# Kernel optimization log

Measured on AMD Instinct MI355X. Metric: run time of the kernel, lower is better.

## Reference

```python
import jax, jax.numpy as jnp
import numpy as np

N_QUBITS = 8
N_LAYERS = 4
DIM = 2 ** N_QUBITS
C64 = jnp.complex64
ROTS = ['RX', 'RY', 'RZ']

# PauliZ sign table: wire 0 is the most-significant bit (PennyLane convention).
_bits = (np.arange(DIM)[:, None] >> (N_QUBITS - 1 - np.arange(N_QUBITS))[None, :]) & 1
Z_SIGNS = jnp.asarray(1.0 - 2.0 * _bits, dtype=jnp.float32)  # (DIM, n_qubits)


def _apply_1q(state, gate, q):
    """Apply a 2x2 gate (or batched (B,2,2) gate) on qubit q. state: (B, DIM) complex64."""
    L = 2 ** q
    R = DIM // (2 * L)
    s = state.reshape(-1, L, 2, R)
    if gate.ndim == 3:
        s = jnp.einsum('bij,bljr->blir', gate, s)
    else:
        s = jnp.einsum('ij,bljr->blir', gate, s)
    return s.reshape(-1, DIM)


def _apply_cnot(state, q):
    """CNOT with control q, target q+1 (adjacent wires): permute basis states."""
    L = 2 ** q
    R = DIM // (4 * L)
    perm = jnp.array([0, 1, 3, 2])
    s = state.reshape(-1, L, 4, R)[:, :, perm, :]
    return s.reshape(-1, DIM)


def _rot(name, t):
    """Scalar-angle single-qubit rotation gate, 2x2 complex64."""
    h = 0.5 * t
    c = jnp.cos(h).astype(C64)
    s = jnp.sin(h).astype(C64)
    if name == 'RX':
        return jnp.stack([jnp.stack([c, -1j * s]), jnp.stack([-1j * s, c])])
    if name == 'RY':
        return jnp.stack([jnp.stack([c, -s]), jnp.stack([s, c])])
    e = jnp.exp(-1j * h).astype(C64)  # RZ = diag(e^{-it/2}, e^{+it/2})
    z = jnp.zeros((), C64)
    return jnp.stack([jnp.stack([e, z]), jnp.stack([z, jnp.conj(e)])])


def _circuit(enc, theta):
    """enc: (B, n_qubits) real angles; theta: (n_layers, n_qubits, 3). Returns <Z_q>: (B, n_qubits)."""
    B = enc.shape[0]
    state = jnp.zeros((B, DIM), C64).at[:, 0].set(1.0)
    # Angle encoding: RY(enc[:, q]) on each wire (batched gate).
    for q in range(N_QUBITS):
        h = 0.5 * enc[:, q]
        c, s = jnp.cos(h), jnp.sin(h)
        g = jnp.stack([jnp.stack([c, -s], -1), jnp.stack([s, c], -1)], -2).astype(C64)
        state = _apply_1q(state, g, q)
    # PCE ansatz: per layer RX/RY/RZ on every qubit, then brickwall CNOT entanglement.
    for l in range(N_LAYERS):
        for q in range(N_QUBITS):
            for r, name in enumerate(ROTS):
                state = _apply_1q(state, _rot(name, theta[l, q, r]), q)
        for i in range(l % 2, N_QUBITS - 1, 2):
            state = _apply_cnot(state, i)
    probs = state.real ** 2 + state.imag ** 2          # (B, DIM)
    return probs @ Z_SIGNS                              # (B, n_qubits)


def setup_inputs() -> dict:
    key = jax.random.key(0)
    k1, k2, k3, k4 = jax.random.split(key, 4)
    B, D_IN, D_OUT = 8192, 512, 512
    x = jax.random.normal(k1, (B, D_IN), dtype=jnp.float32)
    W_in = jax.random.normal(k2, (N_QUBITS, D_IN), dtype=jnp.float32) * (1.0 / np.sqrt(D_IN))
    W_out = jax.random.normal(k3, (D_OUT, N_QUBITS), dtype=jnp.float32) * (1.0 / np.sqrt(N_QUBITS))
    theta = jax.random.normal(k4, (N_LAYERS, N_QUBITS, 3), dtype=jnp.float32) * 0.1
    return {"x": x, "W_in": W_in, "W_out": W_out, "theta": theta}


def reference(x, W_in, W_out, theta):
    enc = jnp.tanh(x @ W_in.T) * jnp.pi     # (B, n_qubits), encoded angles
    z = _circuit(enc, theta)                # (B, n_qubits), PauliZ expvals
    return z @ W_out.T                      # (B, output_dim)
```

## Files before the change

### kernel.cpp

```cpp
#include <hip/hip_runtime.h>
#include <hip/hip_bf16.h>
#include <math.h>


typedef __attribute__((ext_vector_type(8))) short bf16x8;
typedef __attribute__((ext_vector_type(4))) float f32x4;

__device__ __forceinline__ float2 shfl_xor_f2(float2 v, int m) {
  float2 r;
  r.x = __shfl_xor(v.x, m, 64);
  r.y = __shfl_xor(v.y, m, 64);
  return r;
}
__device__ __forceinline__ float2 cfma(float2 u, float2 v, float2 acc) {
  acc.x = fmaf(u.x, v.x, fmaf(-u.y, v.y, acc.x));
  acc.y = fmaf(u.x, v.y, fmaf(u.y, v.x, acc.y));
  return acc;
}

__device__ __forceinline__ void apply_gate(float2 (&a)[4], int q, float2 u00,
                                           float2 u01, float2 u10, float2 u11,
                                           int lane) {
  const float2 z0 = make_float2(0.f, 0.f);
  if (q == 7) {
    float2 n0 = cfma(u00, a[0], cfma(u01, a[1], z0));
    float2 n1 = cfma(u10, a[0], cfma(u11, a[1], z0));
    float2 n2 = cfma(u00, a[2], cfma(u01, a[3], z0));
    float2 n3 = cfma(u10, a[2], cfma(u11, a[3], z0));
    a[0] = n0; a[1] = n1; a[2] = n2; a[3] = n3;
  } else if (q == 6) {
    float2 n0 = cfma(u00, a[0], cfma(u01, a[2], z0));
    float2 n2 = cfma(u10, a[0], cfma(u11, a[2], z0));
    float2 n1 = cfma(u00, a[1], cfma(u01, a[3], z0));
    float2 n3 = cfma(u10, a[1], cfma(u11, a[3], z0));
    a[0] = n0; a[1] = n1; a[2] = n2; a[3] = n3;
  } else {
    int m = 1 << (5 - q);
    bool b = (lane >> (5 - q)) & 1;
    float2 ca = b ? u11 : u00;
    float2 cp = b ? u10 : u01;
    #pragma unroll
    for (int k = 0; k < 4; ++k) {
      float2 p = shfl_xor_f2(a[k], m);
      a[k] = cfma(ca, a[k], cfma(cp, p, z0));
    }
  }
}

__device__ __forceinline__ void apply_cnot(float2 (&a)[4], int q, int lane) {
  if (q <= 4) {
    int m = 1 << (4 - q);
    bool ctrl = (lane >> (5 - q)) & 1;
    #pragma unroll
    for (int k = 0; k < 4; ++k) {
      float2 p = shfl_xor_f2(a[k], m);
      a[k].x = ctrl ? p.x : a[k].x;
      a[k].y = ctrl ? p.y : a[k].y;
    }
  } else if (q == 5) {
    bool ct = lane & 1;
    float2 n0 = ct ? a[2] : a[0];
    float2 n1 = ct ? a[3] : a[1];
    float2 n2 = ct ? a[0] : a[2];
    float2 n3 = ct ? a[1] : a[3];
    a[0] = n0; a[1] = n1; a[2] = n2; a[3] = n3;
  } else {
    float2 t = a[2]; a[2] = a[3]; a[3] = t;
  }
}

__global__ __launch_bounds__(256) void k01_kernel(
    const float* __restrict__ x, const float* __restrict__ W_in,
    const float* __restrict__ theta, __hip_bfloat16* __restrict__ Bt,
    __hip_bfloat16* __restrict__ psi, int psi_stride, int B) {
  __shared__ float mats[32 * 8];
  const int tid = threadIdx.x;
  const int lane = tid & 63;

  if (blockIdx.x < 64) {
    if (tid < 32) {
      int l = tid >> 3, q = tid & 7;
      const float* th = theta + (l * 8 + q) * 3;
      float h1 = 0.5f * th[0], h2 = 0.5f * th[1], h3 = 0.5f * th[2];
      float c1 = cosf(h1), s1 = sinf(h1);
      float c2 = cosf(h2), s2 = sinf(h2);
      float c3 = cosf(h3), s3 = sinf(h3);
      float m00r = c2 * c1, m00i = s2 * s1;
      float m01r = -s2 * c1, m01i = -c2 * s1;
      float m10r = s2 * c1, m10i = -c2 * s1;
      float m11r = c1 * c2, m11i = -s1 * s2;
      float* o = &mats[tid * 8];
      o[0] = c3 * m00r + s3 * m00i;  o[1] = c3 * m00i - s3 * m00r;
      o[2] = c3 * m01r + s3 * m01i;  o[3] = c3 * m01i - s3 * m01r;
      o[4] = c3 * m10r - s3 * m10i;  o[5] = c3 * m10i + s3 * m10r;
      o[6] = c3 * m11r - s3 * m11i;  o[7] = c3 * m11i + s3 * m11r;
    }
    __syncthreads();

    const int j = blockIdx.x * 4 + (tid >> 6);
    float2 a[4];
    #pragma unroll
    for (int k = 0; k < 4; ++k)
      a[k] = make_float2((lane * 4 + k == j) ? 1.f : 0.f, 0.f);

    #pragma unroll
    for (int l = 0; l < 4; ++l) {
      #pragma unroll
      for (int q = 0; q < 8; ++q) {
        const float* m = &mats[(l * 8 + q) * 8];
        float2 u00 = make_float2(m[0], m[1]);
        float2 u01 = make_float2(m[2], m[3]);
        float2 u10 = make_float2(m[4], m[5]);
        float2 u11 = make_float2(m[6], m[7]);
        apply_gate(a, q, u00, u01, u10, u11, lane);
      }
      #pragma unroll
      for (int i = (l & 1); i < 7; i += 2) apply_cnot(a, i, lane);
    }
    #pragma unroll
    for (int k = 0; k < 4; ++k) {
      int n0 = (lane * 4 + k) * 2;
      Bt[n0 * 256 + j]       = __float2bfloat16(a[k].x);
      Bt[(n0 + 1) * 256 + j] = __float2bfloat16(a[k].y);
    }
    return;
  }

  const int b = (int)(blockIdx.x - 64) * 4 + (tid >> 6);
  if (b >= B) return;

  float xv[8];
  #pragma unroll
  for (int j = 0; j < 8; ++j) xv[j] = x[b * 512 + j * 64 + lane];

  float acc[8];
  #pragma unroll
  for (int q = 0; q < 8; ++q) {
    float s = 0.f;
    #pragma unroll
    for (int j = 0; j < 8; ++j)
      s = fmaf(xv[j], W_in[q * 512 + j * 64 + lane], s);
    acc[q] = s;
  }
  #pragma unroll
  for (int m = 1; m < 64; m <<= 1) {
    #pragma unroll
    for (int q = 0; q < 8; ++q) acc[q] += __shfl_xor(acc[q], m, 64);
  }

  float cq[8], sq[8];
  #pragma unroll
  for (int q = 0; q < 8; ++q) {
    float e  = __expf(2.f * acc[q]);
    float th = 1.f - __fdividef(2.f, e + 1.f);
    float h  = 0.5f * 3.14159265358979323846f * th;
    cq[q] = __cosf(h);
    sq[q] = __sinf(h);
  }

  float base = 1.f;
  #pragma unroll
  for (int q = 0; q < 6; ++q)
    base *= ((lane >> (5 - q)) & 1) ? sq[q] : cq[q];

  float a0 = base * cq[6] * cq[7];
  float a1 = base * cq[6] * sq[7];
  float a2 = base * sq[6] * cq[7];
  float a3 = base * sq[6] * sq[7];

  __hip_bfloat16 h4[4] = {__float2bfloat16(a0), __float2bfloat16(a1),
                          __float2bfloat16(a2), __float2bfloat16(a3)};
  uint2 pk = *reinterpret_cast<uint2*>(h4);
  *reinterpret_cast<uint2*>(psi + (size_t)b * psi_stride + lane * 4) = pk;
}

__global__ __launch_bounds__(256, 1) void k2_kernel(
    const __hip_bfloat16* __restrict__ psi, const __hip_bfloat16* __restrict__ Bt,
    const float* __restrict__ W_out, float* __restrict__ out, int psi_stride) {
  __shared__ float z_lds[4][32][8];
  __shared__ float z_final[32][8];
  const int tid = threadIdx.x;
  const int lane = tid & 63;
  const int w = tid >> 6;
  const int rowbase = blockIdx.x * 32;
  const int cl = lane & 15;
  const int kg = lane >> 4;

  const short* psis = (const short*)psi;
  const short* Bts  = (const short*)Bt;

  bf16x8 Af[2][8];
  #pragma unroll
  for (int rt = 0; rt < 2; ++rt)
    #pragma unroll
    for (int kb = 0; kb < 8; ++kb)
      Af[rt][kb] = *(const bf16x8*)(psis +
          (size_t)(rowbase + rt * 16 + cl) * psi_stride + kb * 32 + kg * 8);

  const int wcol = w * 128;
  f32x4 acc[2][8];
  #pragma unroll
  for (int rt = 0; rt < 2; ++rt)
    #pragma unroll
    for (int ct = 0; ct < 8; ++ct) acc[rt][ct] = (f32x4){0.f, 0.f, 0.f, 0.f};

  #pragma unroll
  for (int ct = 0; ct < 8; ++ct) {
    const short* bp = Bts + (size_t)(wcol + ct * 16 + cl) * 256 + kg * 8;
    bf16x8 Bf[8];
    #pragma unroll
    for (int kb = 0; kb < 8; ++kb) Bf[kb] = *(const bf16x8*)(bp + kb * 32);
    #pragma unroll
    for (int kb = 0; kb < 8; ++kb) {
      acc[0][ct] = __builtin_amdgcn_mfma_f32_16x16x32_bf16(Af[0][kb], Bf[kb],
                                                           acc[0][ct], 0, 0, 0);
      acc[1][ct] = __builtin_amdgcn_mfma_f32_16x16x32_bf16(Af[1][kb], Bf[kb],
                                                           acc[1][ct], 0, 0, 0);
    }
  }

  float zacc[2][4][4];
  #pragma unroll
  for (int rt = 0; rt < 2; ++rt)
    #pragma unroll
    for (int u = 0; u < 4; ++u)
      #pragma unroll
      for (int jr = 0; jr < 4; ++jr) zacc[rt][u][jr] = 0.f;

  #pragma unroll
  for (int ct = 0; ct < 8; ++ct) {
    int n = wcol + ct * 16 + cl;
    int i = n >> 1;
    int ib = (lane & 1) ? (i & 15) : (i >> 4);
    float s[4];
    #pragma unroll
    for (int u = 0; u < 4; ++u)
      s[u] = ((ib >> (3 - u)) & 1) ? -1.f : 1.f;
    #pragma unroll
    for (int rt = 0; rt < 2; ++rt) {
      #pragma unroll
      for (int jr = 0; jr < 4; ++jr) {
        float v = acc[rt][ct][jr];
        v = v * v;
        float P = v + __shfl_xor(v, 1, 64);
        #pragma unroll
        for (int u = 0; u < 4; ++u)
          zacc[rt][u][jr] = fmaf(s[u], P, zacc[rt][u][jr]);
      }
    }
  }

  #pragma unroll
  for (int m = 2; m <= 8; m <<= 1)
    #pragma unroll
    for (int rt = 0; rt < 2; ++rt)
      #pragma unroll
      for (int u = 0; u < 4; ++u)
        #pragma unroll
        for (int jr = 0; jr < 4; ++jr)
          zacc[rt][u][jr] += __shfl_xor(zacc[rt][u][jr], m, 64);

  if (cl <= 1) {
    #pragma unroll
    for (int rt = 0; rt < 2; ++rt)
      #pragma unroll
      for (int u = 0; u < 4; ++u)
        #pragma unroll
        for (int jr = 0; jr < 4; ++jr)
          z_lds[w][rt * 16 + kg * 4 + jr][(lane & 1) * 4 + u] = zacc[rt][u][jr];
  }
  __syncthreads();

  {
    int r = tid >> 3, q = tid & 7;
    z_final[r][q] = z_lds[0][r][q] + z_lds[1][r][q] + z_lds[2][r][q] +
                    z_lds[3][r][q];
  }
  __syncthreads();

  const int o0 = tid, o1 = 256 + tid;
  float4 wa0 = *(const float4*)(W_out + o0 * 8);
  float4 wb0 = *(const float4*)(W_out + o0 * 8 + 4);
  float4 wa1 = *(const float4*)(W_out + o1 * 8);
  float4 wb1 = *(const float4*)(W_out + o1 * 8 + 4);
  #pragma unroll 4
  for (int r = 0; r < 32; ++r) {
    float4 z0 = *(const float4*)&z_final[r][0];
    float4 z1 = *(const float4*)&z_final[r][4];
    float d0 = wa0.x * z0.x + wa0.y * z0.y + wa0.z * z0.z + wa0.w * z0.w +
               wb0.x * z1.x + wb0.y * z1.y + wb0.z * z1.z + wb0.w * z1.w;
    float d1 = wa1.x * z0.x + wa1.y * z0.y + wa1.z * z0.z + wa1.w * z0.w +
               wb1.x * z1.x + wb1.y * z1.y + wb1.z * z1.z + wb1.w * z1.w;
    out[(size_t)(rowbase + r) * 512 + o0] = d0;
    out[(size_t)(rowbase + r) * 512 + o1] = d1;
  }
}

extern "C" void kernel_launch(void* const* d_in, const int* in_sizes, int n_in,
                              void* d_out, int out_size, void* d_ws, size_t ws_size,
                              hipStream_t stream) {
  const float* x     = (const float*)d_in[0];
  const float* W_in  = (const float*)d_in[1];
  const float* W_out = (const float*)d_in[2];
  const float* theta = (const float*)d_in[3];
  float* out = (float*)d_out;

  const int B = in_sizes[0] / 512;
  const size_t btBytes  = 512 * 256 * sizeof(__hip_bfloat16);
  const size_t psiBytes = (size_t)B * 256 * sizeof(__hip_bfloat16);

  __hip_bfloat16* Bt = (__hip_bfloat16*)d_ws;
  __hip_bfloat16* psi;
  int psi_stride;
  if (ws_size >= btBytes + psiBytes) {
    psi = (__hip_bfloat16*)((char*)d_ws + btBytes);
    psi_stride = 256;
  } else {
    psi = (__hip_bfloat16*)d_out;
    psi_stride = 1024;
  }

  hipLaunchKernelGGL(k01_kernel, dim3(64 + B / 4), dim3(256), 0, stream,
                     x, W_in, theta, Bt, psi, psi_stride, B);
  hipLaunchKernelGGL(k2_kernel, dim3(B / 32), dim3(256), 0, stream,
                     psi, Bt, W_out, out, psi_stride);
}
```

Measured before the change: 35.28 us.

## Fuse encoding into MFMA kernel via LDS psi staging, split unitary kernel

The psi encoding (x·W_in, tanh, product state) now runs inside the MFMA kernel and stages psi in a swizzled LDS tile, so psi no longer round-trips through global memory. The unitary build moves to its own small 64-block kernel. Row tiles drop from 32 to 16 per block with launch bounds allowing 2 blocks per SM, and output stores become float2. The trade-off is that each block reloads W_in and B-matrix fragments for fewer rows, and k1 now runs serially before k2 instead of concurrently with the encoding work.

```diff
diff --git a/kernel.cpp b/kernel.cpp
--- a/kernel.cpp
+++ b/kernel.cpp
@@ -69,163 +69,152 @@
   }
 }
 
-__global__ __launch_bounds__(256) void k01_kernel(
-    const float* __restrict__ x, const float* __restrict__ W_in,
-    const float* __restrict__ theta, __hip_bfloat16* __restrict__ Bt,
-    __hip_bfloat16* __restrict__ psi, int psi_stride, int B) {
+__global__ __launch_bounds__(256) void k1_unitary(
+    const float* __restrict__ theta, __hip_bfloat16* __restrict__ Bt) {
   __shared__ float mats[32 * 8];
   const int tid = threadIdx.x;
   const int lane = tid & 63;
 
-  if (blockIdx.x < 64) {
-    if (tid < 32) {
-      int l = tid >> 3, q = tid & 7;
-      const float* th = theta + (l * 8 + q) * 3;
-      float h1 = 0.5f * th[0], h2 = 0.5f * th[1], h3 = 0.5f * th[2];
-      float c1 = cosf(h1), s1 = sinf(h1);
-      float c2 = cosf(h2), s2 = sinf(h2);
-      float c3 = cosf(h3), s3 = sinf(h3);
-      float m00r = c2 * c1, m00i = s2 * s1;
-      float m01r = -s2 * c1, m01i = -c2 * s1;
-      float m10r = s2 * c1, m10i = -c2 * s1;
-      float m11r = c1 * c2, m11i = -s1 * s2;
-      float* o = &mats[tid * 8];
-      o[0] = c3 * m00r + s3 * m00i;  o[1] = c3 * m00i - s3 * m00r;
-      o[2] = c3 * m01r + s3 * m01i;  o[3] = c3 * m01i - s3 * m01r;
-      o[4] = c3 * m10r - s3 * m10i;  o[5] = c3 * m10i + s3 * m10r;
-      o[6] = c3 * m11r - s3 * m11i;  o[7] = c3 * m11i + s3 * m11r;
-    }
-    __syncthreads();
-
-    const int j = blockIdx.x * 4 + (tid >> 6);
-    float2 a[4];
-    #pragma unroll
-    for (int k = 0; k < 4; ++k)
-      a[k] = make_float2((lane * 4 + k == j) ? 1.f : 0.f, 0.f);
-
-    #pragma unroll
-    for (int l = 0; l < 4; ++l) {
-      #pragma unroll
-      for (int q = 0; q < 8; ++q) {
-        const float* m = &mats[(l * 8 + q) * 8];
-        float2 u00 = make_float2(m[0], m[1]);
-        float2 u01 = make_float2(m[2], m[3]);
-        float2 u10 = make_float2(m[4], m[5]);
-        float2 u11 = make_float2(m[6], m[7]);
-        apply_gate(a, q, u00, u01, u10, u11, lane);
-      }
-      #pragma unroll
-      for (int i = (l & 1); i < 7; i += 2) apply_cnot(a, i, lane);
-    }
-    #pragma unroll
-    for (int k = 0; k < 4; ++k) {
-      int n0 = (lane * 4 + k) * 2;
-      Bt[n0 * 256 + j]       = __float2bfloat16(a[k].x);
-      Bt[(n0 + 1) * 256 + j] = __float2bfloat16(a[k].y);
-    }
-    return;
-  }
-
-  const int b = (int)(blockIdx.x - 64) * 4 + (tid >> 6);
-  if (b >= B) return;
-
-  float xv[8];
-  #pragma unroll
-  for (int j = 0; j < 8; ++j) xv[j] = x[b * 512 + j * 64 + lane];
-
-  float acc[8];
-  #pragma unroll
-  for (int q = 0; q < 8; ++q) {
-    float s = 0.f;
-    #pragma unroll
-    for (int j = 0; j < 8; ++j)
-      s = fmaf(xv[j], W_in[q * 512 + j * 64 + lane], s);
-    acc[q] = s;
-  }
-  #pragma unroll
-  for (int m = 1; m < 64; m <<= 1) {
-    #pragma unroll
-    for (int q = 0; q < 8; ++q) acc[q] += __shfl_xor(acc[q], m, 64);
-  }
-
-  float cq[8], sq[8];
-  #pragma unroll
-  for (int q = 0; q < 8; ++q) {
-    float e  = __expf(2.f * acc[q]);
-    float th = 1.f - __fdividef(2.f, e + 1.f);
-    float h  = 0.5f * 3.14159265358979323846f * th;
-    cq[q] = __cosf(h);
-    sq[q] = __sinf(h);
-  }
-
-  float base = 1.f;
-  #pragma unroll
-  for (int q = 0; q < 6; ++q)
-    base *= ((lane >> (5 - q)) & 1) ? sq[q] : cq[q];
-
-  float a0 = base * cq[6] * cq[7];
-  float a1 = base * cq[6] * sq[7];
-  float a2 = base * sq[6] * cq[7];
-  float a3 = base * sq[6] * sq[7];
-
-  __hip_bfloat16 h4[4] = {__float2bfloat16(a0), __float2bfloat16(a1),
-                          __float2bfloat16(a2), __float2bfloat16(a3)};
-  uint2 pk = *reinterpret_cast<uint2*>(h4);
-  *reinterpret_cast<uint2*>(psi + (size_t)b * psi_stride + lane * 4) = pk;
-}
-
-__global__ __launch_bounds__(256, 1) void k2_kernel(
-    const __hip_bfloat16* __restrict__ psi, const __hip_bfloat16* __restrict__ Bt,
-    const float* __restrict__ W_out, float* __restrict__ out, int psi_stride) {
-  __shared__ float z_lds[4][32][8];
-  __shared__ float z_final[32][8];
+  if (tid < 32) {
+    int l = tid >> 3, q = tid & 7;
+    const float* th = theta + (l * 8 + q) * 3;
+    float h1 = 0.5f * th[0], h2 = 0.5f * th[1], h3 = 0.5f * th[2];
+    float c1 = cosf(h1), s1 = sinf(h1);
+    float c2 = cosf(h2), s2 = sinf(h2);
+    float c3 = cosf(h3), s3 = sinf(h3);
+    float m00r = c2 * c1, m00i = s2 * s1;
+    float m01r = -s2 * c1, m01i = -c2 * s1;
+    float m10r = s2 * c1, m10i = -c2 * s1;
+    float m11r = c1 * c2, m11i = -s1 * s2;
+    float* o = &mats[tid * 8];
+    o[0] = c3 * m00r + s3 * m00i;  o[1] = c3 * m00i - s3 * m00r;
+    o[2] = c3 * m01r + s3 * m01i;  o[3] = c3 * m01i - s3 * m01r;
+    o[4] = c3 * m10r - s3 * m10i;  o[5] = c3 * m10i + s3 * m10r;
+    o[6] = c3 * m11r - s3 * m11i;  o[7] = c3 * m11i + s3 * m11r;
+  }
+  __syncthreads();
+
+  const int j = blockIdx.x * 4 + (tid >> 6);
+  float2 a[4];
+  #pragma unroll
+  for (int k = 0; k < 4; ++k)
+    a[k] = make_float2((lane * 4 + k == j) ? 1.f : 0.f, 0.f);
+
+  #pragma unroll
+  for (int l = 0; l < 4; ++l) {
+    #pragma unroll
+    for (int q = 0; q < 8; ++q) {
+      const float* m = &mats[(l * 8 + q) * 8];
+      float2 u00 = make_float2(m[0], m[1]);
+      float2 u01 = make_float2(m[2], m[3]);
+      float2 u10 = make_float2(m[4], m[5]);
+      float2 u11 = make_float2(m[6], m[7]);
+      apply_gate(a, q, u00, u01, u10, u11, lane);
+    }
+    #pragma unroll
+    for (int i = (l & 1); i < 7; i += 2) apply_cnot(a, i, lane);
+  }
+  #pragma unroll
+  for (int k = 0; k < 4; ++k) {
+    int n0 = (lane * 4 + k) * 2;
+    Bt[n0 * 256 + j]       = __float2bfloat16(a[k].x);
+    Bt[(n0 + 1) * 256 + j] = __float2bfloat16(a[k].y);
+  }
+}
+
+__global__ __launch_bounds__(256, 2) void k2_fused(
+    const float* __restrict__ x, const float* __restrict__ W_in,
+    const float* __restrict__ W_out, const __hip_bfloat16* __restrict__ Bt,
+    float* __restrict__ out) {
+  __shared__ char psi_lds[16 * 512];
+  __shared__ float z_lds[4][16][8];
+  __shared__ float z_final[16][8];
+
   const int tid = threadIdx.x;
   const int lane = tid & 63;
   const int w = tid >> 6;
-  const int rowbase = blockIdx.x * 32;
+  const int rowbase = blockIdx.x * 16;
+
+  const float4* W4 = (const float4*)W_in;
+  float4 Wa[8], Wb[8];
+  #pragma unroll
+  for (int q = 0; q < 8; ++q) {
+    Wa[q] = W4[q * 128 + lane];
+    Wb[q] = W4[q * 128 + 64 + lane];
+  }
+
+  #pragma unroll
+  for (int rr = 0; rr < 4; ++rr) {
+    const int r = w * 4 + rr;
+    const float4* x4 = (const float4*)(x + (size_t)(rowbase + r) * 512);
+    float4 xa = x4[lane], xb = x4[64 + lane];
+    float acc[8];
+    #pragma unroll
+    for (int q = 0; q < 8; ++q) {
+      acc[q] = xa.x * Wa[q].x + xa.y * Wa[q].y + xa.z * Wa[q].z + xa.w * Wa[q].w +
+               xb.x * Wb[q].x + xb.y * Wb[q].y + xb.z * Wb[q].z + xb.w * Wb[q].w;
+    }
+    #pragma unroll
+    for (int m = 1; m < 64; m <<= 1)
+      #pragma unroll
+      for (int q = 0; q < 8; ++q) acc[q] += __shfl_xor(acc[q], m, 64);
+
+    float cq[8], sq[8];
+    #pragma unroll
+    for (int q = 0; q < 8; ++q) {
+      float e  = __expf(2.f * acc[q]);
+      float th = 1.f - __fdividef(2.f, e + 1.f);
+      float h  = 1.57079632679489662f * th;
+      cq[q] = __cosf(h);
+      sq[q] = __sinf(h);
+    }
+    float base = 1.f;
+    #pragma unroll
+    for (int q = 0; q < 6; ++q)
+      base *= ((lane >> (5 - q)) & 1) ? sq[q] : cq[q];
+
+    __hip_bfloat16 h4[4];
+    h4[0] = __float2bfloat16(base * cq[6] * cq[7]);
+    h4[1] = __float2bfloat16(base * cq[6] * sq[7]);
+    h4[2] = __float2bfloat16(base * sq[6] * cq[7]);
+    h4[3] = __float2bfloat16(base * sq[6] * sq[7]);
+    int byte = r * 512 + ((lane * 8) ^ ((r & 7) << 4));
+    *(uint2*)(psi_lds + byte) = *(uint2*)h4;
+  }
+  __syncthreads();
+
   const int cl = lane & 15;
   const int kg = lane >> 4;
-
-  const short* psis = (const short*)psi;
-  const short* Bts  = (const short*)Bt;
-
-  bf16x8 Af[2][8];
-  #pragma unroll
-  for (int rt = 0; rt < 2; ++rt)
-    #pragma unroll
-    for (int kb = 0; kb < 8; ++kb)
-      Af[rt][kb] = *(const bf16x8*)(psis +
-          (size_t)(rowbase + rt * 16 + cl) * psi_stride + kb * 32 + kg * 8);
-
   const int wcol = w * 128;
-  f32x4 acc[2][8];
-  #pragma unroll
-  for (int rt = 0; rt < 2; ++rt)
-    #pragma unroll
-    for (int ct = 0; ct < 8; ++ct) acc[rt][ct] = (f32x4){0.f, 0.f, 0.f, 0.f};
-
-  #pragma unroll
-  for (int ct = 0; ct < 8; ++ct) {
-    const short* bp = Bts + (size_t)(wcol + ct * 16 + cl) * 256 + kg * 8;
-    bf16x8 Bf[8];
-    #pragma unroll
-    for (int kb = 0; kb < 8; ++kb) Bf[kb] = *(const bf16x8*)(bp + kb * 32);
-    #pragma unroll
-    for (int kb = 0; kb < 8; ++kb) {
-      acc[0][ct] = __builtin_amdgcn_mfma_f32_16x16x32_bf16(Af[0][kb], Bf[kb],
-                                                           acc[0][ct], 0, 0, 0);
-      acc[1][ct] = __builtin_amdgcn_mfma_f32_16x16x32_bf16(Af[1][kb], Bf[kb],
-                                                           acc[1][ct], 0, 0, 0);
-    }
-  }
-
-  float zacc[2][4][4];
-  #pragma unroll
-  for (int rt = 0; rt < 2; ++rt)
-    #pragma unroll
-    for (int u = 0; u < 4; ++u)
-      #pragma unroll
-      for (int jr = 0; jr < 4; ++jr) zacc[rt][u][jr] = 0.f;
+
+  bf16x8 Af[8];
+  #pragma unroll
+  for (int kb = 0; kb < 8; ++kb) {
+    int byte = cl * 512 + ((kg * 16 + kb * 64) ^ ((cl & 7) << 4));
+    Af[kb] = *(const bf16x8*)(psi_lds + byte);
+  }
+
+  f32x4 acc2[8];
+  #pragma unroll
+  for (int ct = 0; ct < 8; ++ct) acc2[ct] = (f32x4){0.f, 0.f, 0.f, 0.f};
+
+  const short* Bts = (const short*)Bt;
+  #pragma unroll
+  for (int kb = 0; kb < 8; ++kb) {
+    #pragma unroll
+    for (int ct = 0; ct < 8; ++ct) {
+      bf16x8 bf = *(const bf16x8*)(Bts +
+          (size_t)(wcol + ct * 16 + cl) * 256 + kg * 8 + kb * 32);
+      acc2[ct] = __builtin_amdgcn_mfma_f32_16x16x32_bf16(Af[kb], bf,
+                                                         acc2[ct], 0, 0, 0);
+    }
+  }
+
+  float zacc[4][4];
+  #pragma unroll
+  for (int u = 0; u < 4; ++u)
+    #pragma unroll
+    for (int jr = 0; jr < 4; ++jr) zacc[u][jr] = 0.f;
 
   #pragma unroll
   for (int ct = 0; ct < 8; ++ct) {
@@ -237,62 +226,55 @@
     for (int u = 0; u < 4; ++u)
       s[u] = ((ib >> (3 - u)) & 1) ? -1.f : 1.f;
     #pragma unroll
-    for (int rt = 0; rt < 2; ++rt) {
-      #pragma unroll
-      for (int jr = 0; jr < 4; ++jr) {
-        float v = acc[rt][ct][jr];
-        v = v * v;
-        float P = v + __shfl_xor(v, 1, 64);
-        #pragma unroll
-        for (int u = 0; u < 4; ++u)
-          zacc[rt][u][jr] = fmaf(s[u], P, zacc[rt][u][jr]);
-      }
+    for (int jr = 0; jr < 4; ++jr) {
+      float v = acc2[ct][jr];
+      v = v * v;
+      float P = v + __shfl_xor(v, 1, 64);
+      #pragma unroll
+      for (int u = 0; u < 4; ++u)
+        zacc[u][jr] = fmaf(s[u], P, zacc[u][jr]);
     }
   }
 
   #pragma unroll
   for (int m = 2; m <= 8; m <<= 1)
     #pragma unroll
-    for (int rt = 0; rt < 2; ++rt)
-      #pragma unroll
-      for (int u = 0; u < 4; ++u)
-        #pragma unroll
-        for (int jr = 0; jr < 4; ++jr)
-          zacc[rt][u][jr] += __shfl_xor(zacc[rt][u][jr], m, 64);
+    for (int u = 0; u < 4; ++u)
+      #pragma unroll
+      for (int jr = 0; jr < 4; ++jr)
+        zacc[u][jr] += __shfl_xor(zacc[u][jr], m, 64);
 
   if (cl <= 1) {
     #pragma unroll
-    for (int rt = 0; rt < 2; ++rt)
-      #pragma unroll
-      for (int u = 0; u < 4; ++u)
-        #pragma unroll
-        for (int jr = 0; jr < 4; ++jr)
-          z_lds[w][rt * 16 + kg * 4 + jr][(lane & 1) * 4 + u] = zacc[rt][u][jr];
-  }
-  __syncthreads();
-
-  {
+    for (int u = 0; u < 4; ++u)
+      #pragma unroll
+      for (int jr = 0; jr < 4; ++jr)
+        z_lds[w][kg * 4 + jr][(lane & 1) * 4 + u] = zacc[u][jr];
+  }
+  __syncthreads();
+
+  if (tid < 128) {
     int r = tid >> 3, q = tid & 7;
     z_final[r][q] = z_lds[0][r][q] + z_lds[1][r][q] + z_lds[2][r][q] +
                     z_lds[3][r][q];
   }
   __syncthreads();
 
-  const int o0 = tid, o1 = 256 + tid;
-  float4 wa0 = *(const float4*)(W_out + o0 * 8);
-  float4 wb0 = *(const float4*)(W_out + o0 * 8 + 4);
-  float4 wa1 = *(const float4*)(W_out + o1 * 8);
-  float4 wb1 = *(const float4*)(W_out + o1 * 8 + 4);
+  const int o0 = tid * 2;
+  float4 wa0 = *(const float4*)(W_out + (size_t)o0 * 8);
+  float4 wb0 = *(const float4*)(W_out + (size_t)o0 * 8 + 4);
+  float4 wa1 = *(const float4*)(W_out + (size_t)o0 * 8 + 8);
+  float4 wb1 = *(const float4*)(W_out + (size_t)o0 * 8 + 12);
   #pragma unroll 4
-  for (int r = 0; r < 32; ++r) {
+  for (int r = 0; r < 16; ++r) {
     float4 z0 = *(const float4*)&z_final[r][0];
     float4 z1 = *(const float4*)&z_final[r][4];
-    float d0 = wa0.x * z0.x + wa0.y * z0.y + wa0.z * z0.z + wa0.w * z0.w +
-               wb0.x * z1.x + wb0.y * z1.y + wb0.z * z1.z + wb0.w * z1.w;
-    float d1 = wa1.x * z0.x + wa1.y * z0.y + wa1.z * z0.z + wa1.w * z0.w +
-               wb1.x * z1.x + wb1.y * z1.y + wb1.z * z1.z + wb1.w * z1.w;
-    out[(size_t)(rowbase + r) * 512 + o0] = d0;
-    out[(size_t)(rowbase + r) * 512 + o1] = d1;
+    float2 d;
+    d.x = wa0.x * z0.x + wa0.y * z0.y + wa0.z * z0.z + wa0.w * z0.w +
+          wb0.x * z1.x + wb0.y * z1.y + wb0.z * z1.z + wb0.w * z1.w;
+    d.y = wa1.x * z0.x + wa1.y * z0.y + wa1.z * z0.z + wa1.w * z0.w +
+          wb1.x * z1.x + wb1.y * z1.y + wb1.z * z1.z + wb1.w * z1.w;
+    *(float2*)(out + (size_t)(rowbase + r) * 512 + o0) = d;
   }
 }
 
@@ -306,22 +288,9 @@
   float* out = (float*)d_out;
 
   const int B = in_sizes[0] / 512;
-  const size_t btBytes  = 512 * 256 * sizeof(__hip_bfloat16);
-  const size_t psiBytes = (size_t)B * 256 * sizeof(__hip_bfloat16);
-
   __hip_bfloat16* Bt = (__hip_bfloat16*)d_ws;
-  __hip_bfloat16* psi;
-  int psi_stride;
-  if (ws_size >= btBytes + psiBytes) {
-    psi = (__hip_bfloat16*)((char*)d_ws + btBytes);
-    psi_stride = 256;
-  } else {
-    psi = (__hip_bfloat16*)d_out;
-    psi_stride = 1024;
-  }
-
-  hipLaunchKernelGGL(k01_kernel, dim3(64 + B / 4), dim3(256), 0, stream,
-                     x, W_in, theta, Bt, psi, psi_stride, B);
-  hipLaunchKernelGGL(k2_kernel, dim3(B / 32), dim3(256), 0, stream,
-                     psi, Bt, W_out, out, psi_stride);
-}
+
+  hipLaunchKernelGGL(k1_unitary, dim3(64), dim3(256), 0, stream, theta, Bt);
+  hipLaunchKernelGGL(k2_fused, dim3(B / 16), dim3(256), 0, stream,
+                     x, W_in, W_out, Bt, out);
+}
```

Measured after the change: 43.41 us. 1.23x slower.

## Split k2 across eight waves per block with 512 threads

Applied to the files above, without the earlier changes.

Doubles the k2 block to 512 threads so each wave handles 64 output columns of the unitary matmul instead of 128. Each wave now needs only half the accumulators, and B fragments are loaded per (kb, ct) inside the MFMA loop instead of being staged eight at a time. The LDS reduction grows to eight partial slices, and each thread writes one output column. The aim is more waves in flight and lower register pressure per wave, at the cost of every block reloading its A fragments in twice as many waves and a larger cross-wave reduction. A cosmetic constant fold in k01 is also included.

```diff
diff --git a/kernel.cpp b/kernel.cpp
--- a/kernel.cpp
+++ b/kernel.cpp
@@ -153,7 +153,7 @@
   for (int q = 0; q < 8; ++q) {
     float e  = __expf(2.f * acc[q]);
     float th = 1.f - __fdividef(2.f, e + 1.f);
-    float h  = 0.5f * 3.14159265358979323846f * th;
+    float h  = 1.57079632679489662f * th;
     cq[q] = __cosf(h);
     sq[q] = __sinf(h);
   }
@@ -174,10 +174,10 @@
   *reinterpret_cast<uint2*>(psi + (size_t)b * psi_stride + lane * 4) = pk;
 }
 
-__global__ __launch_bounds__(256, 1) void k2_kernel(
+__global__ __launch_bounds__(512, 2) void k2_kernel(
     const __hip_bfloat16* __restrict__ psi, const __hip_bfloat16* __restrict__ Bt,
     const float* __restrict__ W_out, float* __restrict__ out, int psi_stride) {
-  __shared__ float z_lds[4][32][8];
+  __shared__ float z_lds[8][32][8];
   __shared__ float z_final[32][8];
   const int tid = threadIdx.x;
   const int lane = tid & 63;
@@ -185,6 +185,7 @@
   const int rowbase = blockIdx.x * 32;
   const int cl = lane & 15;
   const int kg = lane >> 4;
+  const int wcol = w * 64;
 
   const short* psis = (const short*)psi;
   const short* Bts  = (const short*)Bt;
@@ -197,25 +198,22 @@
       Af[rt][kb] = *(const bf16x8*)(psis +
           (size_t)(rowbase + rt * 16 + cl) * psi_stride + kb * 32 + kg * 8);
 
-  const int wcol = w * 128;
-  f32x4 acc[2][8];
+  f32x4 acc2[2][4];
   #pragma unroll
   for (int rt = 0; rt < 2; ++rt)
     #pragma unroll
-    for (int ct = 0; ct < 8; ++ct) acc[rt][ct] = (f32x4){0.f, 0.f, 0.f, 0.f};
-
-  #pragma unroll
-  for (int ct = 0; ct < 8; ++ct) {
-    const short* bp = Bts + (size_t)(wcol + ct * 16 + cl) * 256 + kg * 8;
-    bf16x8 Bf[8];
-    #pragma unroll
-    for (int kb = 0; kb < 8; ++kb) Bf[kb] = *(const bf16x8*)(bp + kb * 32);
-    #pragma unroll
-    for (int kb = 0; kb < 8; ++kb) {
-      acc[0][ct] = __builtin_amdgcn_mfma_f32_16x16x32_bf16(Af[0][kb], Bf[kb],
-                                                           acc[0][ct], 0, 0, 0);
-      acc[1][ct] = __builtin_amdgcn_mfma_f32_16x16x32_bf16(Af[1][kb], Bf[kb],
-                                                           acc[1][ct], 0, 0, 0);
+    for (int ct = 0; ct < 4; ++ct) acc2[rt][ct] = (f32x4){0.f, 0.f, 0.f, 0.f};
+
+  #pragma unroll
+  for (int kb = 0; kb < 8; ++kb) {
+    #pragma unroll
+    for (int ct = 0; ct < 4; ++ct) {
+      bf16x8 bf = *(const bf16x8*)(Bts +
+          (size_t)(wcol + ct * 16 + cl) * 256 + kg * 8 + kb * 32);
+      acc2[0][ct] = __builtin_amdgcn_mfma_f32_16x16x32_bf16(Af[0][kb], bf,
+                                                            acc2[0][ct], 0, 0, 0);
+      acc2[1][ct] = __builtin_amdgcn_mfma_f32_16x16x32_bf16(Af[1][kb], bf,
+                                                            acc2[1][ct], 0, 0, 0);
     }
   }
 
@@ -228,7 +226,7 @@
       for (int jr = 0; jr < 4; ++jr) zacc[rt][u][jr] = 0.f;
 
   #pragma unroll
-  for (int ct = 0; ct < 8; ++ct) {
+  for (int ct = 0; ct < 4; ++ct) {
     int n = wcol + ct * 16 + cl;
     int i = n >> 1;
     int ib = (lane & 1) ? (i & 15) : (i >> 4);
@@ -240,7 +238,7 @@
     for (int rt = 0; rt < 2; ++rt) {
       #pragma unroll
       for (int jr = 0; jr < 4; ++jr) {
-        float v = acc[rt][ct][jr];
+        float v = acc2[rt][ct][jr];
         v = v * v;
         float P = v + __shfl_xor(v, 1, 64);
         #pragma unroll
@@ -271,28 +269,24 @@
   }
   __syncthreads();
 
-  {
+  if (tid < 256) {
     int r = tid >> 3, q = tid & 7;
-    z_final[r][q] = z_lds[0][r][q] + z_lds[1][r][q] + z_lds[2][r][q] +
-                    z_lds[3][r][q];
+    float s = 0.f;
+    #pragma unroll
+    for (int wv = 0; wv < 8; ++wv) s += z_lds[wv][r][q];
+    z_final[r][q] = s;
   }
   __syncthreads();
 
-  const int o0 = tid, o1 = 256 + tid;
-  float4 wa0 = *(const float4*)(W_out + o0 * 8);
-  float4 wb0 = *(const float4*)(W_out + o0 * 8 + 4);
-  float4 wa1 = *(const float4*)(W_out + o1 * 8);
-  float4 wb1 = *(const float4*)(W_out + o1 * 8 + 4);
+  float4 wa = *(const float4*)(W_out + (size_t)tid * 8);
+  float4 wb = *(const float4*)(W_out + (size_t)tid * 8 + 4);
   #pragma unroll 4
   for (int r = 0; r < 32; ++r) {
     float4 z0 = *(const float4*)&z_final[r][0];
     float4 z1 = *(const float4*)&z_final[r][4];
-    float d0 = wa0.x * z0.x + wa0.y * z0.y + wa0.z * z0.z + wa0.w * z0.w +
-               wb0.x * z1.x + wb0.y * z1.y + wb0.z * z1.z + wb0.w * z1.w;
-    float d1 = wa1.x * z0.x + wa1.y * z0.y + wa1.z * z0.z + wa1.w * z0.w +
-               wb1.x * z1.x + wb1.y * z1.y + wb1.z * z1.z + wb1.w * z1.w;
-    out[(size_t)(rowbase + r) * 512 + o0] = d0;
-    out[(size_t)(rowbase + r) * 512 + o1] = d1;
+    float d = wa.x * z0.x + wa.y * z0.y + wa.z * z0.z + wa.w * z0.w +
+              wb.x * z1.x + wb.y * z1.y + wb.z * z1.z + wb.w * z1.w;
+    out[(size_t)(rowbase + r) * 512 + tid] = d;
   }
 }
 
@@ -322,6 +316,6 @@
 
   hipLaunchKernelGGL(k01_kernel, dim3(64 + B / 4), dim3(256), 0, stream,
                      x, W_in, theta, Bt, psi, psi_stride, B);
-  hipLaunchKernelGGL(k2_kernel, dim3(B / 32), dim3(256), 0, stream,
+  hipLaunchKernelGGL(k2_kernel, dim3(B / 32), dim3(512), 0, stream,
                      psi, Bt, W_out, out, psi_stride);
 }
```

Result: no change. 35.84 us (+1.6%).
